# Kernel optimization log

Hardware: AMD Instinct MI355X
Metric: run time of the kernel (lower is better)

Reference implementation:

```python
import jax, jax.numpy as jnp
import numpy as np

N_RES = 500000


def _rot(vals):
    # stack 9 scalars-per-element into (..., 3, 3) row-major rotation matrices
    return jnp.stack(vals, axis=-1).reshape(*vals[0].shape, 3, 3)


def _dihedral(p0, p1, p2, p3):
    b0 = -(p1 - p0)
    b1 = p2 - p1
    b2 = p3 - p2
    b0xb1 = jnp.cross(b0, b1)
    b1xb2 = jnp.cross(b2, b1)
    y = jnp.sum(jnp.cross(b0xb1, b1xb2) * b1, axis=-1) / jnp.linalg.norm(b1, axis=-1)
    x = jnp.sum(b0xb1 * b1xb2, axis=-1)
    return jnp.nan_to_num(jnp.arctan2(y, x))


def _bb_dihedrals(N, CA, C):
    phi_ = _dihedral(C[:-1], N[1:], CA[1:], C[1:])
    psi_ = _dihedral(N[:-1], CA[:-1], C[:-1], N[1:])
    omg_ = _dihedral(CA[:-1], C[:-1], N[1:], CA[1:])
    pad = jnp.zeros_like(phi_[:1])
    omega = jnp.concatenate([omg_, pad])
    phi = jnp.concatenate([pad, phi_])
    psi = jnp.concatenate([psi_, pad])
    return jnp.stack([omega, phi, psi], axis=-1)  # (n, 3)


def _frames_from_reference(n_xyz, ca_xyz, c_xyz, eps=1e-20):
    # OpenFold Rigid.make_transform_from_reference
    n = n_xyz - ca_xyz
    c = c_xyz - ca_xyz
    cx, cy, cz = c[..., 0], c[..., 1], c[..., 2]
    z = jnp.zeros_like(cx)
    o = jnp.ones_like(cx)
    nrm = jnp.sqrt(eps + cx**2 + cy**2)
    s1, c1 = -cy / nrm, cx / nrm
    R1 = _rot([c1, -s1, z, s1, c1, z, z, z, o])
    nrm2 = jnp.sqrt(eps + cx**2 + cy**2 + cz**2)
    s2, c2 = cz / nrm2, jnp.sqrt(cx**2 + cy**2) / nrm2
    R2 = _rot([c2, z, s2, z, o, z, -s2, z, c2])
    Rc = R2 @ R1
    n2 = jnp.einsum('...ij,...j->...i', Rc, n)
    ny, nz_ = n2[..., 1], n2[..., 2]
    nrm3 = jnp.sqrt(eps + ny**2 + nz_**2)
    sn, cn = -nz_ / nrm3, ny / nrm3
    Rn = _rot([o, z, z, z, cn, -sn, z, sn, cn])
    rots = jnp.swapaxes(Rn @ Rc, -1, -2)
    return rots, ca_xyz  # (n,3,3), (n,3)


def _compose(ra, ta, rb, tb):
    # rigid composition: (ra,ta) o (rb,tb)
    return ra @ rb, jnp.einsum('...ij,...j->...i', ra, tb) + ta


def _forward(aa, bb_coords, sc_torsions, default_frames, group_idx, atom_mask, lit_positions):
    n_xyz, ca_xyz, c_xyz = bb_coords[:, 0], bb_coords[:, 1], bb_coords[:, 2]
    bb_r, bb_t = _frames_from_reference(n_xyz, ca_xyz, c_xyz)

    angles = jnp.concatenate([_bb_dihedrals(n_xyz, ca_xyz, c_xyz), sc_torsions], axis=-1)  # (n,7)
    alpha = jnp.stack([jnp.sin(angles), jnp.cos(angles)], axis=-1)  # (n,7,2) [sin, cos]
    bb_pad = jnp.concatenate([
        jnp.zeros((alpha.shape[0], 1, 1), alpha.dtype),
        jnp.ones((alpha.shape[0], 1, 1), alpha.dtype)], axis=-1)
    alpha = jnp.concatenate([bb_pad, alpha], axis=-2)  # (n,8,2)

    # torsion_angles_to_frames
    d4 = default_frames[aa]            # (n,8,4,4)
    dr, dt = d4[..., :3, :3], d4[..., :3, 3]
    s, cA = alpha[..., 0], alpha[..., 1]
    z = jnp.zeros_like(s)
    o = jnp.ones_like(s)
    Ra = _rot([o, z, z, z, cA, -s, z, s, cA])  # (n,8,3,3) x-axis rotation
    fr = dr @ Ra
    ft = dt
    # chain chi2->chi1, chi3->chi2, chi4->chi3
    r2, t2 = _compose(fr[:, 4], ft[:, 4], fr[:, 5], ft[:, 5])
    r3, t3 = _compose(r2, t2, fr[:, 6], ft[:, 6])
    r4, t4 = _compose(r3, t3, fr[:, 7], ft[:, 7])
    all_r = jnp.concatenate([fr[:, :5], r2[:, None], r3[:, None], r4[:, None]], axis=1)
    all_t = jnp.concatenate([ft[:, :5], t2[:, None], t3[:, None], t4[:, None]], axis=1)
    gr, gt = _compose(bb_r[:, None], bb_t[:, None], all_r, all_t)  # (n,8,3,3), (n,8,3)

    # frames_and_literature_positions_to_atom14_pos (one-hot sum == gather)
    n = aa.shape[0]
    g = group_idx[aa]                   # (n,14)
    ridx = jnp.arange(n)[:, None]
    ar = gr[ridx, g]                    # (n,14,3,3)
    at = gt[ridx, g]                    # (n,14,3)
    lit = lit_positions[aa]             # (n,14,3)
    pred = jnp.einsum('naij,naj->nai', ar, lit) + at
    pred = pred * atom_mask[aa][..., None]

    # use_native_bb_coords=True: keep input backbone atoms
    return jnp.concatenate([bb_coords, pred[:, 4:]], axis=1)  # (n,14,3)


def setup_inputs() -> dict:
    key = jax.random.key(0)
    ks = jax.random.split(key, 7)
    n = N_RES
    aa = jax.random.randint(ks[0], (n,), 0, 21, dtype=jnp.int32)
    bb_coords = jax.random.normal(ks[1], (n, 4, 3), jnp.float32) * 3.0
    sc_torsions = jax.random.uniform(ks[2], (n, 4), jnp.float32, -np.pi, np.pi)
    default_frames = jax.random.normal(ks[3], (21, 8, 4, 4), jnp.float32)
    group_idx = jax.random.randint(ks[4], (21, 14), 0, 8, dtype=jnp.int32)
    atom_mask = (jax.random.uniform(ks[5], (21, 14)) > 0.2).astype(jnp.float32)
    lit_positions = jax.random.normal(ks[6], (21, 14, 3), jnp.float32)
    return {"aa": aa, "bb_coords": bb_coords, "sc_torsions": sc_torsions,
            "default_frames": default_frames, "group_idx": group_idx,
            "atom_mask": atom_mask, "lit_positions": lit_positions}


def reference(aa, bb_coords, sc_torsions, default_frames, group_idx, atom_mask, lit_positions):
    return _forward(aa, bb_coords, sc_torsions, default_frames, group_idx, atom_mask, lit_positions)
```

## Files before the change

### kernel.cpp

```cpp
#include <hip/hip_runtime.h>
#include <hip/hip_fp16.h>


struct F3 { float x, y, z; };

__device__ __forceinline__ F3 f3sub(F3 a, F3 b) { return {a.x-b.x, a.y-b.y, a.z-b.z}; }
__device__ __forceinline__ F3 f3cross(F3 a, F3 b) {
    return {a.y*b.z - a.z*b.y, a.z*b.x - a.x*b.z, a.x*b.y - a.y*b.x};
}
__device__ __forceinline__ float f3dot(F3 a, F3 b) { return a.x*b.x + a.y*b.y + a.z*b.z; }

__device__ __forceinline__ void dihedral_from(F3 A, F3 B, F3 mid,
                                              float& s, float& c) {
    float x = f3dot(A, B);
    F3 w = f3cross(A, B);
    float y = f3dot(w, mid) * rsqrtf(fmaxf(f3dot(mid, mid), 1e-30f));
    float r2 = x * x + y * y;
    float rinv = rsqrtf(r2);
    bool ok = r2 > 1e-24f;
    s = ok ? y * rinv : 0.0f;
    c = ok ? x * rinv : 1.0f;
}

struct Xf12 { float m[9]; float t[3]; };
__device__ __forceinline__ Xf12 mk_fr(float4 r0, float4 r1, float4 r2,
                                      float sA, float cA) {
    Xf12 o;
    o.m[0] = r0.x; o.m[1] = fmaf(cA, r0.y, sA * r0.z); o.m[2] = fmaf(cA, r0.z, -sA * r0.y);
    o.m[3] = r1.x; o.m[4] = fmaf(cA, r1.y, sA * r1.z); o.m[5] = fmaf(cA, r1.z, -sA * r1.y);
    o.m[6] = r2.x; o.m[7] = fmaf(cA, r2.y, sA * r2.z); o.m[8] = fmaf(cA, r2.z, -sA * r2.y);
    o.t[0] = r0.w; o.t[1] = r1.w; o.t[2] = r2.w;
    return o;
}

__device__ __forceinline__ void cond_apply(const Xf12& F, bool cond,
                                           float& qx, float& qy, float& qz) {
    float tx = fmaf(F.m[0], qx, fmaf(F.m[1], qy, fmaf(F.m[2], qz, F.t[0])));
    float ty = fmaf(F.m[3], qx, fmaf(F.m[4], qy, fmaf(F.m[5], qz, F.t[1])));
    float tz = fmaf(F.m[6], qx, fmaf(F.m[7], qy, fmaf(F.m[8], qz, F.t[2])));
    qx = cond ? tx : qx; qy = cond ? ty : qy; qz = cond ? tz : qz;
}

__device__ __forceinline__ unsigned pkh(float a, float b) {
    __half2 h = __floats2half2_rn(a, b);
    return *reinterpret_cast<unsigned*>(&h);
}
__device__ __forceinline__ float2 h2fu(unsigned u) {
    __half2 h = *reinterpret_cast<__half2*>(&u);
    return __half22float2(h);
}

#define OT_STRIDE 27
#define AUV_AA    84

__global__ __launch_bounds__(256)
__attribute__((amdgpu_waves_per_eu(2, 4)))
void idealizer_kernel(
    const int*   __restrict__ aa,
    const float* __restrict__ bb,
    const float* __restrict__ tor,
    const float* __restrict__ dframes,
    const int*   __restrict__ gidx,
    const float* __restrict__ amask,
    const float* __restrict__ lit,
    float*       __restrict__ out,
    int n)
{
    __shared__ __align__(8)  unsigned s_ot[256 * OT_STRIDE];
    __shared__ __align__(16) unsigned s_auv[21 * AUV_AA];
    __shared__ unsigned s_gpk[21];
    __shared__ unsigned s_mbit[21];

    const int tid = threadIdx.x;

    if (tid < 210) {
        int aai = (tid * 6554) >> 16;
        int a   = tid - aai * 10;
        int g   = gidx[aai * 14 + 4 + a];
        const float4* dr4 = (const float4*)dframes + (aai * 8 + g) * 4;
        float4 d0 = dr4[0], d1 = dr4[1], d2 = dr4[2];
        const float* lp = lit + aai * 42 + 12 + a * 3;
        float lx = lp[0], ly = lp[1], lz = lp[2];
        float A0 = fmaf(d0.x, lx, d0.w);
        float A1 = fmaf(d1.x, lx, d1.w);
        float A2 = fmaf(d2.x, lx, d2.w);
        float U0 = fmaf(d0.y, ly, d0.z * lz), V0 = fmaf(d0.z, ly, -d0.y * lz);
        float U1 = fmaf(d1.y, ly, d1.z * lz), V1 = fmaf(d1.z, ly, -d1.y * lz);
        float U2 = fmaf(d2.y, ly, d2.z * lz), V2 = fmaf(d2.z, ly, -d2.y * lz);
        unsigned* w = &s_auv[aai * AUV_AA + a * 8];
        *(uint4*)w = make_uint4(pkh(A0, A1), pkh(A2, U0), pkh(U1, U2), pkh(V0, V1));
        w[4] = pkh(V2, 0.0f);
    }
    if (tid < 21) {
        unsigned gp = 0, mb = 0;
        #pragma unroll
        for (int a = 0; a < 10; a++) {
            gp |= ((unsigned)gidx[tid * 14 + 4 + a]) << (3 * a);
            mb |= (amask[tid * 14 + 4 + a] != 0.0f ? 1u : 0u) << a;
        }
        s_gpk[tid] = gp;
        s_mbit[tid] = mb;
    }
    __syncthreads();

    const int i0 = blockIdx.x * 256;
    const int i  = i0 + tid;
    if (i < n) {
        const int aai = aa[i];
        const float4* bb4 = (const float4*)bb;
        float4 q0 = bb4[i * 3 + 0];
        float4 q1 = bb4[i * 3 + 1];
        float4 q2 = bb4[i * 3 + 2];
        const int im = (i > 0)     ? i - 1 : 0;
        const int ip = (i < n - 1) ? i + 1 : 0;
        float4 t1 = bb4[im * 3 + 1];
        float  t2 = bb[im * 12 + 8];
        float4 r0 = bb4[ip * 3 + 0];
        float2 r1 = ((const float2*)bb)[ip * 6 + 2];
        float4 tv = ((const float4*)tor)[i];
        const float4* dfp = (const float4*)dframes + (aai * 32 + 16);
        float4 e40 = dfp[0], e41 = dfp[1],  e42 = dfp[2];
        float4 e50 = dfp[4], e51 = dfp[5],  e52 = dfp[6];
        float4 e60 = dfp[8], e61 = dfp[9],  e62 = dfp[10];

        const unsigned gpk  = s_gpk[aai];
        const unsigned mbit = s_mbit[aai];

        F3 Np  = {q0.x, q0.y, q0.z};
        F3 CAp = {q0.w, q1.x, q1.y};
        F3 Cp  = {q1.z, q1.w, q2.x};
        F3 Cm  = {t1.z, t1.w, t2};
        F3 Nn  = {r0.x, r0.y, r0.z};
        F3 CAn = {r0.w, r1.x, r1.y};

        F3 u1 = f3sub(Np, Cm);
        F3 u2 = f3sub(CAp, Np);
        F3 u3 = f3sub(Cp, CAp);
        F3 u4 = f3sub(Nn, Cp);
        F3 u5 = f3sub(CAn, Nn);
        F3 c12 = f3cross(u1, u2), c23 = f3cross(u2, u3);
        F3 c34 = f3cross(u3, u4), c45 = f3cross(u4, u5);
        float s_ph, c_ph, s_ps, c_ps, s_om, c_om;
        dihedral_from(c12, c23, u2, s_ph, c_ph);
        dihedral_from(c23, c34, u3, s_ps, c_ps);
        dihedral_from(c34, c45, u4, s_om, c_om);
        if (i == 0)     { s_ph = 0.0f; c_ph = 1.0f; }
        if (i == n - 1) { s_ps = 0.0f; c_ps = 1.0f; s_om = 0.0f; c_om = 1.0f; }

        const float eps = 1e-20f;
        F3 nv = f3sub(Np, CAp);
        F3 cv = f3sub(Cp, CAp);
        float cx = cv.x, cy = cv.y, cz2 = cv.z;
        float d2xy  = cx * cx + cy * cy;
        float inrm  = rsqrtf(eps + d2xy);
        float s1 = -cy * inrm, c1 = cx * inrm;
        float inrm2 = rsqrtf(eps + d2xy + cz2 * cz2);
        float s2v = cz2 * inrm2, c2v = sqrtf(d2xy) * inrm2;
        float Rc00 = c2v * c1,  Rc01 = -c2v * s1, Rc02 = s2v;
        float Rc10 = s1,        Rc11 = c1,        Rc12 = 0.0f;
        float Rc20 = -s2v * c1, Rc21 = s2v * s1,  Rc22 = c2v;
        float n2y = Rc10 * nv.x + Rc11 * nv.y + Rc12 * nv.z;
        float n2z = Rc20 * nv.x + Rc21 * nv.y + Rc22 * nv.z;
        float inrm3 = rsqrtf(eps + n2y * n2y + n2z * n2z);
        float sn = -n2z * inrm3, cn = n2y * inrm3;
        float M10 = cn * Rc10 - sn * Rc20, M11 = cn * Rc11 - sn * Rc21, M12 = cn * Rc12 - sn * Rc22;
        float M20 = sn * Rc10 + cn * Rc20, M21 = sn * Rc11 + cn * Rc21;
        float M22 = sn * Rc12 + cn * Rc22;
        float B00 = Rc00, B01 = M10, B02 = M20;
        float B10 = Rc01, B11 = M11, B12 = M21;
        float B20 = Rc02, B21 = M12, B22 = M22;

        float sang[8], cang[8];
        sang[0] = 0.0f; cang[0] = 1.0f;
        sang[1] = s_om; cang[1] = c_om;
        sang[2] = s_ph; cang[2] = c_ph;
        sang[3] = s_ps; cang[3] = c_ps;
        __sincosf(tv.x, &sang[4], &cang[4]);
        __sincosf(tv.y, &sang[5], &cang[5]);
        __sincosf(tv.z, &sang[6], &cang[6]);
        __sincosf(tv.w, &sang[7], &cang[7]);

        unsigned* rowd = &s_ot[tid * OT_STRIDE];
        #pragma unroll
        for (int g8 = 0; g8 < 8; g8++)
            rowd[15 + g8] = pkh(sang[g8], cang[g8]);

        const Xf12 F4 = mk_fr(e40, e41, e42, sang[4], cang[4]);
        const Xf12 F5 = mk_fr(e50, e51, e52, sang[5], cang[5]);
        const Xf12 F6 = mk_fr(e60, e61, e62, sang[6], cang[6]);

        const unsigned* auv = &s_auv[aai * AUV_AA];
        float px = 0.0f, py = 0.0f, pz = 0.0f;
        #pragma unroll
        for (int a = 0; a < 10; a++) {
            int g = (gpk >> (3 * a)) & 7;
            float2 sc = h2fu(rowd[15 + g]);
            uint4 rw = *(const uint4*)(auv + a * 8);
            unsigned rv = auv[a * 8 + 4];
            float2 a01  = h2fu(rw.x);
            float2 a2u0 = h2fu(rw.y);
            float2 u12  = h2fu(rw.z);
            float2 v01  = h2fu(rw.w);
            float2 v2_  = h2fu(rv);
            float qx = fmaf(sc.y, a2u0.y, fmaf(sc.x, v01.x, a01.x));
            float qy = fmaf(sc.y, u12.x,  fmaf(sc.x, v01.y, a01.y));
            float qz = fmaf(sc.y, u12.y,  fmaf(sc.x, v2_.x, a2u0.x));
            cond_apply(F6, g >= 7, qx, qy, qz);
            cond_apply(F5, g >= 6, qx, qy, qz);
            cond_apply(F4, g >= 5, qx, qy, qz);
            float mk = ((mbit >> a) & 1u) ? 1.0f : 0.0f;
            float x = mk * fmaf(B00, qx, fmaf(B01, qy, fmaf(B02, qz, CAp.x)));
            float y = mk * fmaf(B10, qx, fmaf(B11, qy, fmaf(B12, qz, CAp.y)));
            float z = mk * fmaf(B20, qx, fmaf(B21, qy, fmaf(B22, qz, CAp.z)));
            if ((a & 1) == 0) {
                px = x; py = y; pz = z;
            } else {
                int base = 3 * (a >> 1);
                rowd[base + 0] = pkh(px, py);
                rowd[base + 1] = pkh(pz, x);
                rowd[base + 2] = pkh(y, z);
            }
        }

        rowd[15] = __float_as_uint(q0.x);
        rowd[16] = __float_as_uint(q0.y);
        rowd[17] = __float_as_uint(q0.z);
        rowd[18] = __float_as_uint(q0.w);
        rowd[19] = __float_as_uint(q1.x);
        rowd[20] = __float_as_uint(q1.y);
        rowd[21] = __float_as_uint(q1.z);
        rowd[22] = __float_as_uint(q1.w);
        rowd[23] = __float_as_uint(q2.x);
        rowd[24] = __float_as_uint(q2.y);
        rowd[25] = __float_as_uint(q2.z);
        rowd[26] = __float_as_uint(q2.w);
    }

    __syncthreads();

    int m = n - i0; if (m > 256) m = 256;
    float2* gout = (float2*)(out + (size_t)i0 * 42);
    if (m == 256) {
        int r = (tid * 24967) >> 19;
        int j = tid - r * 21;
        #pragma unroll
        for (int k = 0; k < 21; k++) {
            int off = tid + (k << 8);
            int base = r * OT_STRIDE;
            unsigned d0 = s_ot[base + ((j < 6) ? (15 + 2 * j) : (j - 6))];
            unsigned d1 = s_ot[base + ((j < 6) ? (16 + 2 * j) : (j - 6))];
            float2 gval = make_float2(__uint_as_float(d0), __uint_as_float(d1));
            float2 lval = h2fu(d0);
            gout[off] = (j < 6) ? gval : lval;
            r += 12; j += 4;
            if (j >= 21) { j -= 21; r += 1; }
        }
    } else {
        const int cnt2 = m * 21;
        int r = tid / 21;
        int j = tid - r * 21;
        for (int off = tid; off < cnt2; off += 256) {
            int base = r * OT_STRIDE;
            unsigned d0 = s_ot[base + ((j < 6) ? (15 + 2 * j) : (j - 6))];
            unsigned d1 = s_ot[base + ((j < 6) ? (16 + 2 * j) : (j - 6))];
            float2 gval = make_float2(__uint_as_float(d0), __uint_as_float(d1));
            float2 lval = h2fu(d0);
            gout[off] = (j < 6) ? gval : lval;
            r += 12; j += 4;
            if (j >= 21) { j -= 21; r += 1; }
        }
    }
}

extern "C" void kernel_launch(void* const* d_in, const int* in_sizes, int n_in,
                              void* d_out, int out_size, void* d_ws, size_t ws_size,
                              hipStream_t stream) {
    const int*   aa  = (const int*)d_in[0];
    const float* bb  = (const float*)d_in[1];
    const float* tor = (const float*)d_in[2];
    const float* df  = (const float*)d_in[3];
    const int*   gi  = (const int*)d_in[4];
    const float* am  = (const float*)d_in[5];
    const float* lp  = (const float*)d_in[6];
    float* outp = (float*)d_out;
    const int n = in_sizes[0];
    const int blocks = (n + 255) / 256;
    idealizer_kernel<<<blocks, 256, 0, stream>>>(aa, bb, tor, df, gi, am, lp, outp, n);
}
```

Baseline: 135.8 us.

## Share neighbor backbone coordinates through LDS instead of redundant global loads

Each thread now writes its own backbone coordinates to shared memory before the barrier and reads the previous and next residue's atoms from neighboring rows. Only the block-edge threads still fetch neighbors from global memory. This removes two redundant global loads per thread. The sin/cos lookup moves from LDS to registers, selected through a branchless mux tree. The default-frame loads are deferred past the barrier, which may lengthen register live ranges and expose their latency.

Result: slower. 147.7 us (+8.8%).

```diff
diff --git a/kernel.cpp b/kernel.cpp
--- a/kernel.cpp
+++ b/kernel.cpp
@@ -48,6 +48,17 @@
 __device__ __forceinline__ float2 h2fu(unsigned u) {
     __half2 h = *reinterpret_cast<__half2*>(&u);
     return __half22float2(h);
+}
+__device__ __forceinline__ float u2f(unsigned u) { return __uint_as_float(u); }
+
+__device__ __forceinline__ unsigned sel8(const unsigned s[8], int g) {
+    unsigned a0 = (g & 1) ? s[1] : s[0];
+    unsigned a1 = (g & 1) ? s[3] : s[2];
+    unsigned a2 = (g & 1) ? s[5] : s[4];
+    unsigned a3 = (g & 1) ? s[7] : s[6];
+    unsigned b0 = (g & 2) ? a1 : a0;
+    unsigned b1 = (g & 2) ? a3 : a2;
+    return (g & 4) ? b1 : b0;
 }
 
 #define OT_STRIDE 27
@@ -101,37 +112,70 @@
         s_gpk[tid] = gp;
         s_mbit[tid] = mb;
     }
-    __syncthreads();
 
     const int i0 = blockIdx.x * 256;
     const int i  = i0 + tid;
+    unsigned* rowd = &s_ot[tid * OT_STRIDE];
+
+    int aai = 0;
+    float4 q0, q1, q2, tv;
+    float4 t1g; float t2g;
+    float4 r0g; float2 r1g;
     if (i < n) {
-        const int aai = aa[i];
+        aai = aa[i];
         const float4* bb4 = (const float4*)bb;
-        float4 q0 = bb4[i * 3 + 0];
-        float4 q1 = bb4[i * 3 + 1];
-        float4 q2 = bb4[i * 3 + 2];
-        const int im = (i > 0)     ? i - 1 : 0;
-        const int ip = (i < n - 1) ? i + 1 : 0;
-        float4 t1 = bb4[im * 3 + 1];
-        float  t2 = bb[im * 12 + 8];
-        float4 r0 = bb4[ip * 3 + 0];
-        float2 r1 = ((const float2*)bb)[ip * 6 + 2];
-        float4 tv = ((const float4*)tor)[i];
-        const float4* dfp = (const float4*)dframes + (aai * 32 + 16);
-        float4 e40 = dfp[0], e41 = dfp[1],  e42 = dfp[2];
-        float4 e50 = dfp[4], e51 = dfp[5],  e52 = dfp[6];
-        float4 e60 = dfp[8], e61 = dfp[9],  e62 = dfp[10];
-
+        q0 = bb4[i * 3 + 0];
+        q1 = bb4[i * 3 + 1];
+        q2 = bb4[i * 3 + 2];
+        tv = ((const float4*)tor)[i];
+        if (tid == 0) {
+            int im = (i > 0) ? i - 1 : 0;
+            t1g = bb4[im * 3 + 1];
+            t2g = bb[im * 12 + 8];
+        }
+        if (tid == 255) {
+            int ip = (i < n - 1) ? i + 1 : 0;
+            r0g = bb4[ip * 3 + 0];
+            r1g = ((const float2*)bb)[ip * 6 + 2];
+        }
+        rowd[15] = __float_as_uint(q0.x);
+        rowd[16] = __float_as_uint(q0.y);
+        rowd[17] = __float_as_uint(q0.z);
+        rowd[18] = __float_as_uint(q0.w);
+        rowd[19] = __float_as_uint(q1.x);
+        rowd[20] = __float_as_uint(q1.y);
+        rowd[21] = __float_as_uint(q1.z);
+        rowd[22] = __float_as_uint(q1.w);
+        rowd[23] = __float_as_uint(q2.x);
+        rowd[24] = __float_as_uint(q2.y);
+        rowd[25] = __float_as_uint(q2.z);
+        rowd[26] = __float_as_uint(q2.w);
+    }
+    __syncthreads();
+
+    if (i < n) {
         const unsigned gpk  = s_gpk[aai];
         const unsigned mbit = s_mbit[aai];
 
         F3 Np  = {q0.x, q0.y, q0.z};
         F3 CAp = {q0.w, q1.x, q1.y};
         F3 Cp  = {q1.z, q1.w, q2.x};
-        F3 Cm  = {t1.z, t1.w, t2};
-        F3 Nn  = {r0.x, r0.y, r0.z};
-        F3 CAn = {r0.w, r1.x, r1.y};
+
+        F3 Cm, Nn, CAn;
+        if (tid > 0) {
+            const unsigned* rm = rowd - OT_STRIDE;
+            Cm = {u2f(rm[21]), u2f(rm[22]), u2f(rm[23])};
+        } else {
+            Cm = {t1g.z, t1g.w, t2g};
+        }
+        if (tid < 255) {
+            const unsigned* rp = rowd + OT_STRIDE;
+            Nn  = {u2f(rp[15]), u2f(rp[16]), u2f(rp[17])};
+            CAn = {u2f(rp[18]), u2f(rp[19]), u2f(rp[20])};
+        } else {
+            Nn  = {r0g.x, r0g.y, r0g.z};
+            CAn = {r0g.w, r1g.x, r1g.y};
+        }
 
         F3 u1 = f3sub(Np, Cm);
         F3 u2 = f3sub(CAp, Np);
@@ -170,6 +214,11 @@
         float B10 = Rc01, B11 = M11, B12 = M21;
         float B20 = Rc02, B21 = M12, B22 = M22;
 
+        const float4* dfp = (const float4*)dframes + (aai * 32 + 16);
+        float4 e40 = dfp[0], e41 = dfp[1],  e42 = dfp[2];
+        float4 e50 = dfp[4], e51 = dfp[5],  e52 = dfp[6];
+        float4 e60 = dfp[8], e61 = dfp[9],  e62 = dfp[10];
+
         float sang[8], cang[8];
         sang[0] = 0.0f; cang[0] = 1.0f;
         sang[1] = s_om; cang[1] = c_om;
@@ -180,10 +229,10 @@
         __sincosf(tv.z, &sang[6], &cang[6]);
         __sincosf(tv.w, &sang[7], &cang[7]);
 
-        unsigned* rowd = &s_ot[tid * OT_STRIDE];
+        unsigned scp[8];
         #pragma unroll
         for (int g8 = 0; g8 < 8; g8++)
-            rowd[15 + g8] = pkh(sang[g8], cang[g8]);
+            scp[g8] = pkh(sang[g8], cang[g8]);
 
         const Xf12 F4 = mk_fr(e40, e41, e42, sang[4], cang[4]);
         const Xf12 F5 = mk_fr(e50, e51, e52, sang[5], cang[5]);
@@ -194,7 +243,7 @@
         #pragma unroll
         for (int a = 0; a < 10; a++) {
             int g = (gpk >> (3 * a)) & 7;
-            float2 sc = h2fu(rowd[15 + g]);
+            float2 sc = h2fu(sel8(scp, g));
             uint4 rw = *(const uint4*)(auv + a * 8);
             unsigned rv = auv[a * 8 + 4];
             float2 a01  = h2fu(rw.x);
@@ -221,19 +270,6 @@
                 rowd[base + 2] = pkh(y, z);
             }
         }
-
-        rowd[15] = __float_as_uint(q0.x);
-        rowd[16] = __float_as_uint(q0.y);
-        rowd[17] = __float_as_uint(q0.z);
-        rowd[18] = __float_as_uint(q0.w);
-        rowd[19] = __float_as_uint(q1.x);
-        rowd[20] = __float_as_uint(q1.y);
-        rowd[21] = __float_as_uint(q1.z);
-        rowd[22] = __float_as_uint(q1.w);
-        rowd[23] = __float_as_uint(q2.x);
-        rowd[24] = __float_as_uint(q2.y);
-        rowd[25] = __float_as_uint(q2.z);
-        rowd[26] = __float_as_uint(q2.w);
     }
 
     __syncthreads();
```
